# Kernel optimization log

Hardware: AMD Instinct MI355X
Metric: run time of the kernel (lower is better)

## Reference

```python
import jax, jax.numpy as jnp
import numpy as np

N = 50000   # nodes
E = 800000  # edges (avg degree 16)
F = 64      # num_features (channels per irrep)
R = 8       # radial basis size
H = 64      # radial MLP hidden
S = 10      # num_species
NPATH = 5   # tensor-product paths: s*Y0->0, s*Y1->1, v*Y0->1, v.Y1->0, v x Y1->1
AVG_NEIGH = 16.0


def setup_inputs() -> dict:
    key = jax.random.key(0)
    ks = jax.random.split(key, 20)
    def w(k, shape, fan_in):
        return jax.random.normal(k, shape, dtype=jnp.float32) / np.sqrt(fan_in)
    return dict(
        vectors=jax.random.normal(ks[0], (E, 3), dtype=jnp.float32),
        node_feats_s=jax.random.normal(ks[1], (N, F), dtype=jnp.float32),
        node_feats_v=jax.random.normal(ks[2], (N, F, 3), dtype=jnp.float32),
        radial_embedding=jax.random.normal(ks[3], (E, R), dtype=jnp.float32),
        Wu_s=w(ks[7], (F, F), F), Wu_v=w(ks[8], (F, F), F),
        W_r1=w(ks[9], (R, H), R), W_r2=w(ks[10], (H, NPATH * F), H),
        Wd_s=w(ks[11], (F, F), F), Wd_v=w(ks[12], (F, F), F),
        w_sym_s=jax.random.normal(ks[13], (S, 3, F), dtype=jnp.float32),
        w_sym_v=jax.random.normal(ks[14], (S, 2, F), dtype=jnp.float32),
        WL_s=w(ks[15], (F, F), F), WL_v=w(ks[16], (F, F), F),
        W_skip_s=w(ks[17], (S, F, F), F), W_skip_v=w(ks[18], (S, F, F), F),
        W_out=w(ks[19], (F, 1), F),
        node_specie=jax.random.randint(ks[4], (N,), 0, S),
        senders=jax.random.randint(ks[5], (E,), 0, N),
        receivers=jax.random.randint(ks[6], (E,), 0, N),
    )


def reference(vectors, node_feats_s, node_feats_v, radial_embedding,
              Wu_s, Wu_v, W_r1, W_r2, Wd_s, Wd_v,
              w_sym_s, w_sym_v, WL_s, WL_v, W_skip_s, W_skip_v, W_out,
              node_specie, senders, receivers):
    n = node_feats_s.shape[0]
    # ---- self-connection: species-indexed linear (skip_tp), per-irrep channel mix
    sc_s = jnp.einsum('nf,nfg->ng', node_feats_s, W_skip_s[node_specie])
    sc_v = jnp.einsum('nfc,nfg->ngc', node_feats_v, W_skip_v[node_specie])
    # ---- InteractionBlock: linear up
    s = node_feats_s @ Wu_s                                  # [N,F]
    v = jnp.einsum('nfc,fg->ngc', node_feats_v, Wu_v)        # [N,F,3]
    # radial MLP -> per-edge, per-path, per-channel tensor-product weights
    h = jax.nn.silu(radial_embedding @ W_r1)
    w = (h @ W_r2).reshape(-1, NPATH, s.shape[1])            # [E,5,F]
    # spherical harmonics (l=1): unit edge vectors
    Y1 = vectors / (jnp.linalg.norm(vectors, axis=-1, keepdims=True) + 1e-9)  # [E,3]
    xs = s[senders]                                          # [E,F]
    xv = v[senders]                                          # [E,F,3]
    # CG tensor product paths (0e+1o) x (Y0+Y1) -> 0e + 1o
    m_s = w[:, 0] * xs + w[:, 3] * jnp.einsum('efc,ec->ef', xv, Y1)
    m_v = (w[:, 1, :, None] * xs[:, :, None] * Y1[:, None, :]
           + w[:, 2, :, None] * xv
           + w[:, 4, :, None] * jnp.cross(xv, Y1[:, None, :]))
    # scatter-sum aggregation over receivers
    agg_s = jax.ops.segment_sum(m_s, receivers, num_segments=n)
    agg_v = jax.ops.segment_sum(m_v, receivers, num_segments=n)
    # linear down to num_features * interaction_irreps
    s = agg_s @ Wd_s
    v = jnp.einsum('nfc,fg->ngc', agg_v, Wd_v)
    # epsilon is None -> divide by sqrt(avg_num_neighbors)
    inv = 1.0 / np.sqrt(AVG_NEIGH).astype(np.float32)
    s = s * inv
    v = v * inv
    # ---- EquivariantProductBasisBlock: symmetric contraction (correlation=2),
    # species-indexed per-channel weights over the symmetric CG basis
    ws = w_sym_s[node_specie]                                # [N,3,F]
    wv = w_sym_v[node_specie]                                # [N,2,F]
    ps = ws[:, 0] * s + ws[:, 1] * s * s + ws[:, 2] * jnp.sum(v * v, axis=-1)
    pv = wv[:, 0, :, None] * v + wv[:, 1, :, None] * (s[:, :, None] * v)
    # linear to num_features * hidden_irreps
    fs = ps @ WL_s
    fv = jnp.einsum('nfc,fg->ngc', pv, WL_v)
    # residual skip connection
    fs = fs + sc_s
    fv = fv + sc_v
    # ---- LinearReadoutBlock to output_irreps = '0e'
    node_outputs = fs @ W_out                                # [N,1]
    return node_outputs, fs, fv
```

## Files before the change

kernel.cpp:

```cpp
#include <hip/hip_runtime.h>
#include <stdint.h>

#define F 64
#define RDIM 8
#define HDIM 64
#define NPATH 5
#define EB 64
#define PADH 72
#define PADN 324
#define NSP 16
#define PB 72
#define NT 4

typedef _Float16 half8 __attribute__((ext_vector_type(8)));
typedef _Float16 half4 __attribute__((ext_vector_type(4)));
typedef float floatx4 __attribute__((ext_vector_type(4)));

__device__ inline half8 h8_from_f32(const float* p) {
    float4 a = ((const float4*)p)[0];
    float4 b = ((const float4*)p)[1];
    half8 h;
    h[0] = (_Float16)a.x; h[1] = (_Float16)a.y; h[2] = (_Float16)a.z; h[3] = (_Float16)a.w;
    h[4] = (_Float16)b.x; h[5] = (_Float16)b.y; h[6] = (_Float16)b.z; h[7] = (_Float16)b.w;
    return h;
}

__device__ inline half8 h8_from_f32_stride3(const float* p) {
    half8 h;
#pragma unroll
    for (int j = 0; j < 8; ++j) h[j] = (_Float16)p[j * 3];
    return h;
}

__device__ inline half8 h8_zero() {
    half8 h;
#pragma unroll
    for (int j = 0; j < 8; ++j) h[j] = (_Float16)0.f;
    return h;
}

__global__ __launch_bounds__(256) void k_pre(
    const float* __restrict__ nfs, const float* __restrict__ nfv,
    const float* __restrict__ Wus, const float* __restrict__ Wuv,
    half4* __restrict__ comb, int N)
{
    __shared__ float4 stage[4][F];
    const int wave = threadIdx.x >> 6, lane = threadIdx.x & 63;
    const int n = blockIdx.x * 4 + wave;
    const bool act = n < N;
    if (act) {
        float xs = nfs[(size_t)n * F + lane];
        const float* pv = nfv + ((size_t)n * F + lane) * 3;
        stage[wave][lane] = make_float4(xs, pv[0], pv[1], pv[2]);
    }
    __syncthreads();
    if (!act) return;
    float as = 0.f, a0 = 0.f, a1 = 0.f, a2 = 0.f;
#pragma unroll 8
    for (int f = 0; f < F; ++f) {
        float4 x = stage[wave][f];
        float ws = Wus[f * F + lane];
        float wv = Wuv[f * F + lane];
        as += x.x * ws; a0 += x.y * wv; a1 += x.z * wv; a2 += x.w * wv;
    }
    half4 o;
    o[0] = (_Float16)as; o[1] = (_Float16)a0; o[2] = (_Float16)a1; o[3] = (_Float16)a2;
    comb[(size_t)n * F + lane] = o;
}

__global__ __launch_bounds__(256) void k_hist(
    const int* __restrict__ recv, int* __restrict__ cnt, int E)
{
    int i = blockIdx.x * 256 + threadIdx.x;
    const int stride = gridDim.x * 256;
    for (; i < E; i += stride) atomicAdd(&cnt[recv[i]], 1);
}

__global__ __launch_bounds__(1024) void k_scanA(
    const int* __restrict__ cnt, int* __restrict__ bsum, int N)
{
    __shared__ int lsum[1024];
    const int tid = threadIdx.x;
    const int i = blockIdx.x * 1024 + tid;
    int x = (i < N) ? cnt[i] : 0;
    lsum[tid] = x;
    __syncthreads();
    for (int off = 512; off > 0; off >>= 1) {
        if (tid < off) lsum[tid] += lsum[tid + off];
        __syncthreads();
    }
    if (tid == 0) bsum[blockIdx.x] = lsum[0];
}

__global__ __launch_bounds__(64) void k_scanB(int* __restrict__ bsum, int nb)
{
    const int lane = threadIdx.x;
    int carry = 0;
    for (int base = 0; base < nb; base += 64) {
        const int idx = base + lane;
        int v = (idx < nb) ? bsum[idx] : 0;
        int incl = v;
#pragma unroll
        for (int off = 1; off < 64; off <<= 1) {
            int u = __shfl_up(incl, off, 64);
            if (lane >= off) incl += u;
        }
        int tot = __shfl(incl, 63, 64);
        if (idx < nb) bsum[idx] = incl - v + carry;
        carry += tot;
    }
}

__global__ __launch_bounds__(1024) void k_scanC(
    const int* __restrict__ cnt, const int* __restrict__ bsum,
    int* __restrict__ cursor, int N)
{
    __shared__ int lsum[1024];
    const int tid = threadIdx.x;
    const int i = blockIdx.x * 1024 + tid;
    int x = (i < N) ? cnt[i] : 0;
    lsum[tid] = x;
    __syncthreads();
    int acc = x;
    for (int off = 1; off < 1024; off <<= 1) {
        int add = (tid >= off) ? lsum[tid - off] : 0;
        __syncthreads();
        acc += add;
        lsum[tid] = acc;
        __syncthreads();
    }
    if (i < N) cursor[i] = acc - x + bsum[blockIdx.x];
}

__global__ __launch_bounds__(256) void k_scatter(
    const int* __restrict__ recv, const int* __restrict__ send,
    int* __restrict__ cursor, int* __restrict__ perm,
    int2* __restrict__ srsort, int E)
{
    int i = blockIdx.x * 256 + threadIdx.x;
    const int stride = gridDim.x * 256;
    for (; i < E; i += stride) {
        int r = recv[i];
        int p = atomicAdd(&cursor[r], 1);
        perm[p] = i;
        srsort[p] = make_int2(send[i], r);
    }
}

__global__ __launch_bounds__(256) void k_nhist(
    const int* __restrict__ specie, int* __restrict__ nbin, int N)
{
    __shared__ int lbin[NSP];
    const int tid = threadIdx.x;
    if (tid < NSP) lbin[tid] = 0;
    __syncthreads();
    const int i = blockIdx.x * 256 + tid;
    if (i < N) atomicAdd(&lbin[specie[i]], 1);
    __syncthreads();
    if (tid < NSP && lbin[tid] > 0) atomicAdd(&nbin[tid], lbin[tid]);
}

__global__ __launch_bounds__(64) void k_nscan(
    const int* __restrict__ nbin, int* __restrict__ ncur)
{
    if (threadIdx.x == 0) {
        int run = 0;
        for (int s = 0; s < NSP; ++s) {
            ncur[s] = run;
            run += ((nbin[s] + 63) >> 6) << 6;
        }
    }
}

__global__ __launch_bounds__(256) void k_nscatter(
    const int* __restrict__ specie, int* __restrict__ ncur,
    int* __restrict__ nperm, int N)
{
    __shared__ int lbin[NSP], lbase[NSP], lcur[NSP];
    const int tid = threadIdx.x;
    if (tid < NSP) { lbin[tid] = 0; lcur[tid] = 0; }
    __syncthreads();
    const int i = blockIdx.x * 256 + tid;
    int sp = -1;
    if (i < N) { sp = specie[i]; atomicAdd(&lbin[sp], 1); }
    __syncthreads();
    if (tid < NSP && lbin[tid] > 0) lbase[tid] = atomicAdd(&ncur[tid], lbin[tid]);
    __syncthreads();
    if (i < N) {
        int off = atomicAdd(&lcur[sp], 1);
        nperm[lbase[sp] + off] = i;
    }
}

__global__ __launch_bounds__(256, 3) void k_edge(
    const float* __restrict__ vecs, const float* __restrict__ re,
    const float* __restrict__ Wr1, const float* __restrict__ Wr2,
    const int* __restrict__ perm, const int2* __restrict__ srsort,
    const half4* __restrict__ comb,
    float* __restrict__ agg_s, float* __restrict__ agg_v, int E)
{
    __shared__ _Float16 h_lds[EB * PADH];
    __shared__ _Float16 w_lds[EB * PADN];
    const int tid = threadIdx.x;
    const int wave = tid >> 6, lane = tid & 63;
    const int l15 = lane & 15, lq = lane >> 4;

    half8 bfrag[5][2];
#pragma unroll
    for (int nt = 0; nt < 5; ++nt)
#pragma unroll
        for (int ks = 0; ks < 2; ++ks)
#pragma unroll
            for (int j = 0; j < 8; ++j) {
                int k = ks * 32 + lq * 8 + j;
                int n = wave * 80 + nt * 16 + l15;
                bfrag[nt][ks][j] = (_Float16)Wr2[k * (NPATH * F) + n];
            }

    float w1r[RDIM];
#pragma unroll
    for (int r = 0; r < RDIM; ++r) w1r[r] = Wr1[r * HDIM + lane];

    const int niter = (E + EB - 1) / EB;
    for (int it = blockIdx.x; it < niter; it += gridDim.x) {
        const int base = it * EB;
        const bool full = (base + EB <= E);

        if (full) {
            const int ew = base + wave * 16;
            int pm[16];
#pragma unroll
            for (int j = 0; j < 4; ++j)
                ((int4*)pm)[j] = ((const int4*)(perm + ew))[j];
            float4 ra[4], rb[4];
#pragma unroll
            for (int j = 0; j < 4; ++j) {
                const float4* rp = (const float4*)(re + (size_t)pm[j] * RDIM);
                ra[j] = rp[0]; rb[j] = rp[1];
            }
#pragma unroll
            for (int t = 0; t < 16; ++t) {
                float4 A = ra[t & 3], B = rb[t & 3];
                if (t < 12) {
                    const float4* rp = (const float4*)(re + (size_t)pm[t + 4] * RDIM);
                    ra[t & 3] = rp[0]; rb[t & 3] = rp[1];
                }
                float h = A.x * w1r[0] + A.y * w1r[1] + A.z * w1r[2] + A.w * w1r[3]
                        + B.x * w1r[4] + B.y * w1r[5] + B.z * w1r[6] + B.w * w1r[7];
                h = h / (1.f + __expf(-h));
                h_lds[(wave * 16 + t) * PADH + lane] = (_Float16)h;
            }
        } else {
            for (int t = 0; t < 16; ++t) {
                const int eloc = wave * 16 + t;
                const int e = base + eloc;
                float h = 0.f;
                if (e < E) {
                    const int pe = perm[e];
                    const float4* rp = (const float4*)(re + (size_t)pe * RDIM);
                    float4 A = rp[0], B = rp[1];
                    h = A.x * w1r[0] + A.y * w1r[1] + A.z * w1r[2] + A.w * w1r[3]
                      + B.x * w1r[4] + B.y * w1r[5] + B.z * w1r[6] + B.w * w1r[7];
                    h = h / (1.f + __expf(-h));
                }
                h_lds[eloc * PADH + lane] = (_Float16)h;
            }
        }
        __syncthreads();

        floatx4 c[4][5];
#pragma unroll
        for (int mt = 0; mt < 4; ++mt)
#pragma unroll
            for (int nt = 0; nt < 5; ++nt)
                c[mt][nt] = (floatx4){0.f, 0.f, 0.f, 0.f};
#pragma unroll
        for (int ks = 0; ks < 2; ++ks) {
            half8 a[4];
#pragma unroll
            for (int mt = 0; mt < 4; ++mt)
                a[mt] = *(const half8*)&h_lds[(mt * 16 + l15) * PADH + ks * 32 + lq * 8];
#pragma unroll
            for (int mt = 0; mt < 4; ++mt)
#pragma unroll
                for (int nt = 0; nt < 5; ++nt)
                    c[mt][nt] = __builtin_amdgcn_mfma_f32_16x16x32_f16(
                        a[mt], bfrag[nt][ks], c[mt][nt], 0, 0, 0);
        }
#pragma unroll
        for (int mt = 0; mt < 4; ++mt)
#pragma unroll
            for (int nt = 0; nt < 5; ++nt)
#pragma unroll
                for (int r = 0; r < 4; ++r) {
                    int row = mt * 16 + lq * 4 + r;
                    int col = wave * 80 + nt * 16 + l15;
                    w_lds[row * PADN + col] = (_Float16)c[mt][nt][r];
                }
        __syncthreads();

        if (full) {
            const int ew = base + wave * 16;
            int pm[16];
            int2 sr[16];
#pragma unroll
            for (int j = 0; j < 4; ++j)
                ((int4*)pm)[j] = ((const int4*)(perm + ew))[j];
#pragma unroll
            for (int j = 0; j < 8; ++j)
                ((int4*)sr)[j] = ((const int4*)(srsort + ew))[j];
            half4 gb[4];
            float vxr[4], vyr[4], vzr[4];
#pragma unroll
            for (int j = 0; j < 4; ++j) {
                gb[j] = comb[(size_t)sr[j].x * F + lane];
                const float* vp = vecs + (size_t)pm[j] * 3;
                vxr[j] = vp[0]; vyr[j] = vp[1]; vzr[j] = vp[2];
            }
            float accs = 0.f, acc0 = 0.f, acc1 = 0.f, acc2 = 0.f;
            int cur = sr[0].y;
#pragma unroll
            for (int t = 0; t < 16; ++t) {
                half4 g = gb[t & 3];
                float vx = vxr[t & 3], vy = vyr[t & 3], vz = vzr[t & 3];
                if (t < 12) {
                    gb[t & 3] = comb[(size_t)sr[t + 4].x * F + lane];
                    const float* vp = vecs + (size_t)pm[t + 4] * 3;
                    vxr[t & 3] = vp[0]; vyr[t & 3] = vp[1]; vzr[t & 3] = vp[2];
                }
                const int eloc = wave * 16 + t;
                float nrm = sqrtf(vx * vx + vy * vy + vz * vz);
                float inv = 1.f / (nrm + 1e-9f);
                float Yx = vx * inv, Yy = vy * inv, Yz = vz * inv;
                float w0  = (float)w_lds[eloc * PADN + 0 * F + lane];
                float w1p = (float)w_lds[eloc * PADN + 1 * F + lane];
                float w2p = (float)w_lds[eloc * PADN + 2 * F + lane];
                float w3p = (float)w_lds[eloc * PADN + 3 * F + lane];
                float w4p = (float)w_lds[eloc * PADN + 4 * F + lane];
                float xs = (float)g[0], x0 = (float)g[1], x1 = (float)g[2], x2 = (float)g[3];
                float dvY = x0 * Yx + x1 * Yy + x2 * Yz;
                float ms = w0 * xs + w3p * dvY;
                float m0 = w1p * xs * Yx + w2p * x0 + w4p * (x1 * Yz - x2 * Yy);
                float m1 = w1p * xs * Yy + w2p * x1 + w4p * (x2 * Yx - x0 * Yz);
                float m2 = w1p * xs * Yz + w2p * x2 + w4p * (x0 * Yy - x1 * Yx);
                if (sr[t].y != cur) {
                    float* asb = agg_s + (size_t)cur * F;
                    float* avb = agg_v + (size_t)cur * 3 * F;
                    unsafeAtomicAdd(&asb[lane], accs);
                    unsafeAtomicAdd(&avb[lane], acc0);
                    unsafeAtomicAdd(&avb[F + lane], acc1);
                    unsafeAtomicAdd(&avb[2 * F + lane], acc2);
                    accs = acc0 = acc1 = acc2 = 0.f;
                    cur = sr[t].y;
                }
                accs += ms; acc0 += m0; acc1 += m1; acc2 += m2;
            }
            {
                float* asb = agg_s + (size_t)cur * F;
                float* avb = agg_v + (size_t)cur * 3 * F;
                unsafeAtomicAdd(&asb[lane], accs);
                unsafeAtomicAdd(&avb[lane], acc0);
                unsafeAtomicAdd(&avb[F + lane], acc1);
                unsafeAtomicAdd(&avb[2 * F + lane], acc2);
            }
        } else {
            for (int t = 0; t < 16; ++t) {
                const int eloc = wave * 16 + t;
                const int e = base + eloc;
                if (e >= E) break;
                const int pe = perm[e];
                const int2 sr = srsort[e];
                const int snd = sr.x, rcv = sr.y;
                const float* vp = vecs + (size_t)pe * 3;
                float vx = vp[0], vy = vp[1], vz = vp[2];
                float nrm = sqrtf(vx * vx + vy * vy + vz * vz);
                float inv = 1.f / (nrm + 1e-9f);
                float Yx = vx * inv, Yy = vy * inv, Yz = vz * inv;
                half4 g = comb[(size_t)snd * F + lane];
                float w0  = (float)w_lds[eloc * PADN + 0 * F + lane];
                float w1p = (float)w_lds[eloc * PADN + 1 * F + lane];
                float w2p = (float)w_lds[eloc * PADN + 2 * F + lane];
                float w3p = (float)w_lds[eloc * PADN + 3 * F + lane];
                float w4p = (float)w_lds[eloc * PADN + 4 * F + lane];
                float xs = (float)g[0], x0 = (float)g[1], x1 = (float)g[2], x2 = (float)g[3];
                float dvY = x0 * Yx + x1 * Yy + x2 * Yz;
                float ms = w0 * xs + w3p * dvY;
                float m0 = w1p * xs * Yx + w2p * x0 + w4p * (x1 * Yz - x2 * Yy);
                float m1 = w1p * xs * Yy + w2p * x1 + w4p * (x2 * Yx - x0 * Yz);
                float m2 = w1p * xs * Yz + w2p * x2 + w4p * (x0 * Yy - x1 * Yx);
                float* asb = agg_s + (size_t)rcv * F;
                float* avb = agg_v + (size_t)rcv * 3 * F;
                unsafeAtomicAdd(&asb[lane], ms);
                unsafeAtomicAdd(&avb[lane], m0);
                unsafeAtomicAdd(&avb[F + lane], m1);
                unsafeAtomicAdd(&avb[2 * F + lane], m2);
            }
        }
    }
}

__global__ __launch_bounds__(256) void k_post_mfma(
    const float* __restrict__ agg_s, const float* __restrict__ agg_v,
    const float* __restrict__ nfs, const float* __restrict__ nfv,
    const float* __restrict__ Wds, const float* __restrict__ Wdv,
    const float* __restrict__ wss, const float* __restrict__ wsv,
    const float* __restrict__ WLs, const float* __restrict__ WLv,
    const float* __restrict__ Wsks, const float* __restrict__ Wskv,
    const float* __restrict__ Wout, const int* __restrict__ specie,
    const int* __restrict__ nperm,
    float* __restrict__ out0, float* __restrict__ out_fs,
    float* __restrict__ out_fv, int N)
{
    __shared__ _Float16 BT[6][64 * PB];
    __shared__ _Float16 P_lds[4][16 * PB];
    const int tid = threadIdx.x;
    const int wave = tid >> 6, lane = tid & 63;
    const int l15 = lane & 15, lq = lane >> 4;
    const int tb0 = blockIdx.x * 64;

    const int nfirst = nperm[tb0];
    const int sp = (nfirst < 0) ? 0 : specie[nfirst];

    {
        const float* srcs[6] = { Wds, Wdv,
                                 Wsks + (size_t)sp * F * F, Wskv + (size_t)sp * F * F,
                                 WLs, WLv };
#pragma unroll
        for (int m = 0; m < 6; ++m) {
            const float* W = srcs[m];
#pragma unroll
            for (int rep = 0; rep < 16; ++rep) {
                int id = rep * 256 + tid;
                int k = id >> 6, n = id & 63;
                BT[m][n * PB + k] = (_Float16)W[k * F + n];
            }
        }
    }
    __syncthreads();

    const int tb = tb0 + wave * 16;
    const int ndA = nperm[tb + l15];
    int ndr[4];
#pragma unroll
    for (int r = 0; r < 4; ++r) ndr[r] = nperm[tb + lq * 4 + r];

#define BFRAG(m, nt, ks) (*(const half8*)&BT[m][((nt) * 16 + l15) * PB + (ks) * 32 + lq * 8])

    floatx4 csk[4][NT];
#pragma unroll
    for (int q = 0; q < 4; ++q)
#pragma unroll
        for (int nt = 0; nt < NT; ++nt) csk[q][nt] = (floatx4){0.f, 0.f, 0.f, 0.f};
#pragma unroll
    for (int ks = 0; ks < 2; ++ks) {
        half8 a_s, a_v0, a_v1, a_v2;
        if (ndA >= 0) {
            a_s  = h8_from_f32(nfs + (size_t)ndA * F + ks * 32 + lq * 8);
            const float* vb = nfv + ((size_t)ndA * F + ks * 32 + lq * 8) * 3;
            a_v0 = h8_from_f32_stride3(vb + 0);
            a_v1 = h8_from_f32_stride3(vb + 1);
            a_v2 = h8_from_f32_stride3(vb + 2);
        } else {
            a_s = a_v0 = a_v1 = a_v2 = h8_zero();
        }
#pragma unroll
        for (int nt = 0; nt < NT; ++nt) {
            half8 bs = BFRAG(2, nt, ks);
            half8 bv = BFRAG(3, nt, ks);
            csk[0][nt] = __builtin_amdgcn_mfma_f32_16x16x32_f16(a_s,  bs, csk[0][nt], 0, 0, 0);
            csk[1][nt] = __builtin_amdgcn_mfma_f32_16x16x32_f16(a_v0, bv, csk[1][nt], 0, 0, 0);
            csk[2][nt] = __builtin_amdgcn_mfma_f32_16x16x32_f16(a_v1, bv, csk[2][nt], 0, 0, 0);
            csk[3][nt] = __builtin_amdgcn_mfma_f32_16x16x32_f16(a_v2, bv, csk[3][nt], 0, 0, 0);
        }
    }

    floatx4 cdn[4][NT];
#pragma unroll
    for (int q = 0; q < 4; ++q)
#pragma unroll
        for (int nt = 0; nt < NT; ++nt) cdn[q][nt] = (floatx4){0.f, 0.f, 0.f, 0.f};
#pragma unroll
    for (int ks = 0; ks < 2; ++ks) {
        half8 a_s, a_v0, a_v1, a_v2;
        if (ndA >= 0) {
            a_s  = h8_from_f32(agg_s + (size_t)ndA * F + ks * 32 + lq * 8);
            const float* vb = agg_v + (size_t)ndA * 3 * F + ks * 32 + lq * 8;
            a_v0 = h8_from_f32(vb);
            a_v1 = h8_from_f32(vb + F);
            a_v2 = h8_from_f32(vb + 2 * F);
        } else {
            a_s = a_v0 = a_v1 = a_v2 = h8_zero();
        }
#pragma unroll
        for (int nt = 0; nt < NT; ++nt) {
            half8 bs = BFRAG(0, nt, ks);
            half8 bv = BFRAG(1, nt, ks);
            cdn[0][nt] = __builtin_amdgcn_mfma_f32_16x16x32_f16(a_s,  bs, cdn[0][nt], 0, 0, 0);
            cdn[1][nt] = __builtin_amdgcn_mfma_f32_16x16x32_f16(a_v0, bv, cdn[1][nt], 0, 0, 0);
            cdn[2][nt] = __builtin_amdgcn_mfma_f32_16x16x32_f16(a_v1, bv, cdn[2][nt], 0, 0, 0);
            cdn[3][nt] = __builtin_amdgcn_mfma_f32_16x16x32_f16(a_v2, bv, cdn[3][nt], 0, 0, 0);
        }
    }

#pragma unroll
    for (int nt = 0; nt < NT; ++nt) {
        const int g = nt * 16 + l15;
        float a0 = wss[(sp * 3 + 0) * F + g];
        float a1 = wss[(sp * 3 + 1) * F + g];
        float a2 = wss[(sp * 3 + 2) * F + g];
        float b0 = wsv[(sp * 2 + 0) * F + g];
        float b1 = wsv[(sp * 2 + 1) * F + g];
#pragma unroll
        for (int r = 0; r < 4; ++r) {
            const float inv = 0.25f;
            float s2  = cdn[0][nt][r] * inv;
            float v20 = cdn[1][nt][r] * inv;
            float v21 = cdn[2][nt][r] * inv;
            float v22 = cdn[3][nt][r] * inv;
            cdn[0][nt][r] = a0 * s2 + a1 * s2 * s2
                          + a2 * (v20 * v20 + v21 * v21 + v22 * v22);
            cdn[1][nt][r] = b0 * v20 + b1 * s2 * v20;
            cdn[2][nt][r] = b0 * v21 + b1 * s2 * v21;
            cdn[3][nt][r] = b0 * v22 + b1 * s2 * v22;
        }
    }

#pragma unroll
    for (int q = 0; q < 4; ++q) {
#pragma unroll
        for (int nt = 0; nt < NT; ++nt)
#pragma unroll
            for (int r = 0; r < 4; ++r)
                P_lds[wave][(lq * 4 + r) * PB + nt * 16 + l15] = (_Float16)cdn[q][nt][r];
        __syncthreads();
        half8 ap0 = *(const half8*)&P_lds[wave][l15 * PB + 0 * 32 + lq * 8];
        half8 ap1 = *(const half8*)&P_lds[wave][l15 * PB + 1 * 32 + lq * 8];
        const int bm = (q == 0) ? 4 : 5;
#pragma unroll
        for (int nt = 0; nt < NT; ++nt) {
            csk[q][nt] = __builtin_amdgcn_mfma_f32_16x16x32_f16(ap0, BFRAG(bm, nt, 0), csk[q][nt], 0, 0, 0);
            csk[q][nt] = __builtin_amdgcn_mfma_f32_16x16x32_f16(ap1, BFRAG(bm, nt, 1), csk[q][nt], 0, 0, 0);
        }
        __syncthreads();
    }
#undef BFRAG

    float wo[NT];
#pragma unroll
    for (int nt = 0; nt < NT; ++nt) wo[nt] = Wout[nt * 16 + l15];
#pragma unroll
    for (int r = 0; r < 4; ++r) {
        const int nd = ndr[r];
        float po = 0.f;
        if (nd >= 0) {
#pragma unroll
            for (int nt = 0; nt < NT; ++nt) {
                const int g = nt * 16 + l15;
                float fs = csk[0][nt][r];
                out_fs[(size_t)nd * F + g] = fs;
                po += fs * wo[nt];
                float* fvp = out_fv + ((size_t)nd * F + g) * 3;
                fvp[0] = csk[1][nt][r];
                fvp[1] = csk[2][nt][r];
                fvp[2] = csk[3][nt][r];
            }
            po += __shfl_xor(po, 1, 64);
            po += __shfl_xor(po, 2, 64);
            po += __shfl_xor(po, 4, 64);
            po += __shfl_xor(po, 8, 64);
            if (l15 == 0) out0[nd] = po;
        }
    }
}

extern "C" void kernel_launch(void* const* d_in, const int* in_sizes, int n_in,
                              void* d_out, int out_size, void* d_ws, size_t ws_size,
                              hipStream_t stream)
{
    const float* vectors = (const float*)d_in[0];
    const float* nfs  = (const float*)d_in[1];
    const float* nfv  = (const float*)d_in[2];
    const float* re   = (const float*)d_in[3];
    const float* Wus  = (const float*)d_in[4];
    const float* Wuv  = (const float*)d_in[5];
    const float* Wr1  = (const float*)d_in[6];
    const float* Wr2  = (const float*)d_in[7];
    const float* Wds  = (const float*)d_in[8];
    const float* Wdv  = (const float*)d_in[9];
    const float* wss  = (const float*)d_in[10];
    const float* wsv  = (const float*)d_in[11];
    const float* WLs  = (const float*)d_in[12];
    const float* WLv  = (const float*)d_in[13];
    const float* Wsks = (const float*)d_in[14];
    const float* Wskv = (const float*)d_in[15];
    const float* Wout = (const float*)d_in[16];
    const int* specie    = (const int*)d_in[17];
    const int* senders   = (const int*)d_in[18];
    const int* receivers = (const int*)d_in[19];

    const int N = in_sizes[1] / F;
    const int E = in_sizes[18];

    const size_t NF = (size_t)N * F;
    const int NPAD_MAX = N + NSP * 64 + 64;
    half4* comb  = (half4*)d_ws;
    float* agg_s = (float*)((char*)d_ws + NF * sizeof(half4));
    float* agg_v = agg_s + NF;
    int*   perm  = (int*)(agg_v + 3 * NF);
    int2*  srsort = (int2*)(perm + E);
    int*   cnt    = (int*)(srsort + E);
    int*   nbin   = cnt + N;
    int*   ncur   = nbin + NSP;
    int*   cursor = ncur + NSP;
    int*   bsum   = cursor + N;
    int*   nperm  = bsum + 64;

    hipMemsetAsync(agg_s, 0, (size_t)4 * NF * sizeof(float), stream);
    hipMemsetAsync(cnt, 0, (size_t)(N + NSP) * sizeof(int), stream);
    hipMemsetAsync(nperm, 0xFF, (size_t)NPAD_MAX * sizeof(int), stream);

    const int nb = (N + 3) / 4;
    const int nbs = (N + 1023) / 1024;
    const int nb256 = (N + 255) / 256;
    const int nbp = (N + NSP * 64 + 63) / 64;

    k_pre<<<nb, 256, 0, stream>>>(nfs, nfv, Wus, Wuv, comb, N);
    k_hist<<<1024, 256, 0, stream>>>(receivers, cnt, E);
    k_scanA<<<nbs, 1024, 0, stream>>>(cnt, bsum, N);
    k_scanB<<<1, 64, 0, stream>>>(bsum, nbs);
    k_scanC<<<nbs, 1024, 0, stream>>>(cnt, bsum, cursor, N);
    k_scatter<<<1024, 256, 0, stream>>>(receivers, senders, cursor,
                                        perm, srsort, E);
    k_nhist<<<nb256, 256, 0, stream>>>(specie, nbin, N);
    k_nscan<<<1, 64, 0, stream>>>(nbin, ncur);
    k_nscatter<<<nb256, 256, 0, stream>>>(specie, ncur, nperm, N);
    k_edge<<<2048, 256, 0, stream>>>(vectors, re, Wr1, Wr2, perm, srsort,
                                     comb, agg_s, agg_v, E);
    float* out0   = (float*)d_out;
    float* out_fs = out0 + N;
    float* out_fv = out_fs + (size_t)N * F;
    k_post_mfma<<<nbp, 256, 0, stream>>>(agg_s, agg_v, nfs, nfv, Wds, Wdv,
                                         wss, wsv, WLs, WLv, Wsks, Wskv,
                                         Wout, specie, nperm,
                                         out0, out_fs, out_fv, N);
}
```

Before: 600.6 us.

## Use MFMA for the up-projection and fold the species sort into existing kernels

The per-node up-projection, previously a scalar FMA loop with one wave per node, becomes an MFMA f16 kernel. Each wave handles 16 nodes against transposed weights staged in LDS. The species histogram, scan and scatter, previously three separate launches, are folded into the receiver histogram, scanB and edge scatter kernels. This removes launch and small-kernel overhead. The fused node scatter assumes the fixed 1024-block grid covers all N nodes with one thread each.

```diff
diff --git a/kernel.cpp b/kernel.cpp
--- a/kernel.cpp
+++ b/kernel.cpp
@@ -39,41 +39,98 @@
     return h;
 }
 
-__global__ __launch_bounds__(256) void k_pre(
+__global__ __launch_bounds__(256) void k_pre_mfma(
     const float* __restrict__ nfs, const float* __restrict__ nfv,
     const float* __restrict__ Wus, const float* __restrict__ Wuv,
     half4* __restrict__ comb, int N)
 {
-    __shared__ float4 stage[4][F];
-    const int wave = threadIdx.x >> 6, lane = threadIdx.x & 63;
-    const int n = blockIdx.x * 4 + wave;
-    const bool act = n < N;
-    if (act) {
-        float xs = nfs[(size_t)n * F + lane];
-        const float* pv = nfv + ((size_t)n * F + lane) * 3;
-        stage[wave][lane] = make_float4(xs, pv[0], pv[1], pv[2]);
-    }
-    __syncthreads();
-    if (!act) return;
-    float as = 0.f, a0 = 0.f, a1 = 0.f, a2 = 0.f;
-#pragma unroll 8
-    for (int f = 0; f < F; ++f) {
-        float4 x = stage[wave][f];
-        float ws = Wus[f * F + lane];
-        float wv = Wuv[f * F + lane];
-        as += x.x * ws; a0 += x.y * wv; a1 += x.z * wv; a2 += x.w * wv;
-    }
-    half4 o;
-    o[0] = (_Float16)as; o[1] = (_Float16)a0; o[2] = (_Float16)a1; o[3] = (_Float16)a2;
-    comb[(size_t)n * F + lane] = o;
+    __shared__ _Float16 BT[2][64 * PB];
+    const int tid = threadIdx.x;
+    const int wave = tid >> 6, lane = tid & 63;
+    const int l15 = lane & 15, lq = lane >> 4;
+    const int tb0 = blockIdx.x * 64;
+
+    {
+        const float* srcs[2] = { Wus, Wuv };
+#pragma unroll
+        for (int m = 0; m < 2; ++m) {
+            const float* W = srcs[m];
+#pragma unroll
+            for (int rep = 0; rep < 16; ++rep) {
+                int id = rep * 256 + tid;
+                int k = id >> 6, n = id & 63;
+                BT[m][n * PB + k] = (_Float16)W[k * F + n];
+            }
+        }
+    }
+    __syncthreads();
+
+    const int tb = tb0 + wave * 16;
+    const int ndA = tb + l15;
+
+#define BFRAG(m, nt, ks) (*(const half8*)&BT[m][((nt) * 16 + l15) * PB + (ks) * 32 + lq * 8])
+
+    floatx4 c[4][NT];
+#pragma unroll
+    for (int q = 0; q < 4; ++q)
+#pragma unroll
+        for (int nt = 0; nt < NT; ++nt) c[q][nt] = (floatx4){0.f, 0.f, 0.f, 0.f};
+
+#pragma unroll
+    for (int ks = 0; ks < 2; ++ks) {
+        half8 a_s, a_v0, a_v1, a_v2;
+        if (ndA < N) {
+            a_s  = h8_from_f32(nfs + (size_t)ndA * F + ks * 32 + lq * 8);
+            const float* vb = nfv + ((size_t)ndA * F + ks * 32 + lq * 8) * 3;
+            a_v0 = h8_from_f32_stride3(vb + 0);
+            a_v1 = h8_from_f32_stride3(vb + 1);
+            a_v2 = h8_from_f32_stride3(vb + 2);
+        } else {
+            a_s = a_v0 = a_v1 = a_v2 = h8_zero();
+        }
+#pragma unroll
+        for (int nt = 0; nt < NT; ++nt) {
+            half8 bs = BFRAG(0, nt, ks);
+            half8 bv = BFRAG(1, nt, ks);
+            c[0][nt] = __builtin_amdgcn_mfma_f32_16x16x32_f16(a_s,  bs, c[0][nt], 0, 0, 0);
+            c[1][nt] = __builtin_amdgcn_mfma_f32_16x16x32_f16(a_v0, bv, c[1][nt], 0, 0, 0);
+            c[2][nt] = __builtin_amdgcn_mfma_f32_16x16x32_f16(a_v1, bv, c[2][nt], 0, 0, 0);
+            c[3][nt] = __builtin_amdgcn_mfma_f32_16x16x32_f16(a_v2, bv, c[3][nt], 0, 0, 0);
+        }
+    }
+#undef BFRAG
+
+#pragma unroll
+    for (int r = 0; r < 4; ++r) {
+        const int nd = tb + lq * 4 + r;
+        if (nd < N) {
+#pragma unroll
+            for (int nt = 0; nt < NT; ++nt) {
+                half4 o;
+                o[0] = (_Float16)c[0][nt][r];
+                o[1] = (_Float16)c[1][nt][r];
+                o[2] = (_Float16)c[2][nt][r];
+                o[3] = (_Float16)c[3][nt][r];
+                comb[(size_t)nd * F + nt * 16 + l15] = o;
+            }
+        }
+    }
 }
 
 __global__ __launch_bounds__(256) void k_hist(
-    const int* __restrict__ recv, int* __restrict__ cnt, int E)
-{
-    int i = blockIdx.x * 256 + threadIdx.x;
+    const int* __restrict__ recv, int* __restrict__ cnt, int E,
+    const int* __restrict__ specie, int* __restrict__ nbin, int N)
+{
+    __shared__ int lbin[NSP];
+    const int tid = threadIdx.x;
+    if (tid < NSP) lbin[tid] = 0;
+    __syncthreads();
+    const int i0 = blockIdx.x * 256 + tid;
     const int stride = gridDim.x * 256;
-    for (; i < E; i += stride) atomicAdd(&cnt[recv[i]], 1);
+    for (int e = i0; e < E; e += stride) atomicAdd(&cnt[recv[e]], 1);
+    for (int n = i0; n < N; n += stride) atomicAdd(&lbin[specie[n]], 1);
+    __syncthreads();
+    if (tid < NSP && lbin[tid] > 0) atomicAdd(&nbin[tid], lbin[tid]);
 }
 
 __global__ __launch_bounds__(1024) void k_scanA(
@@ -92,7 +149,9 @@
     if (tid == 0) bsum[blockIdx.x] = lsum[0];
 }
 
-__global__ __launch_bounds__(64) void k_scanB(int* __restrict__ bsum, int nb)
+__global__ __launch_bounds__(64) void k_scanB(
+    int* __restrict__ bsum, int nb,
+    const int* __restrict__ nbin, int* __restrict__ ncur)
 {
     const int lane = threadIdx.x;
     int carry = 0;
@@ -108,6 +167,13 @@
         int tot = __shfl(incl, 63, 64);
         if (idx < nb) bsum[idx] = incl - v + carry;
         carry += tot;
+    }
+    if (lane == 0) {
+        int run = 0;
+        for (int s = 0; s < NSP; ++s) {
+            ncur[s] = run;
+            run += ((nbin[s] + 63) >> 6) << 6;
+        }
     }
 }
 
@@ -135,60 +201,30 @@
 __global__ __launch_bounds__(256) void k_scatter(
     const int* __restrict__ recv, const int* __restrict__ send,
     int* __restrict__ cursor, int* __restrict__ perm,
-    int2* __restrict__ srsort, int E)
-{
-    int i = blockIdx.x * 256 + threadIdx.x;
-    const int stride = gridDim.x * 256;
-    for (; i < E; i += stride) {
-        int r = recv[i];
-        int p = atomicAdd(&cursor[r], 1);
-        perm[p] = i;
-        srsort[p] = make_int2(send[i], r);
-    }
-}
-
-__global__ __launch_bounds__(256) void k_nhist(
-    const int* __restrict__ specie, int* __restrict__ nbin, int N)
-{
-    __shared__ int lbin[NSP];
-    const int tid = threadIdx.x;
-    if (tid < NSP) lbin[tid] = 0;
-    __syncthreads();
-    const int i = blockIdx.x * 256 + tid;
-    if (i < N) atomicAdd(&lbin[specie[i]], 1);
-    __syncthreads();
-    if (tid < NSP && lbin[tid] > 0) atomicAdd(&nbin[tid], lbin[tid]);
-}
-
-__global__ __launch_bounds__(64) void k_nscan(
-    const int* __restrict__ nbin, int* __restrict__ ncur)
-{
-    if (threadIdx.x == 0) {
-        int run = 0;
-        for (int s = 0; s < NSP; ++s) {
-            ncur[s] = run;
-            run += ((nbin[s] + 63) >> 6) << 6;
-        }
-    }
-}
-
-__global__ __launch_bounds__(256) void k_nscatter(
+    int2* __restrict__ srsort, int E,
     const int* __restrict__ specie, int* __restrict__ ncur,
     int* __restrict__ nperm, int N)
 {
     __shared__ int lbin[NSP], lbase[NSP], lcur[NSP];
     const int tid = threadIdx.x;
+    const int i0 = blockIdx.x * 256 + tid;
+    const int stride = gridDim.x * 256;
+    for (int e = i0; e < E; e += stride) {
+        int r = recv[e];
+        int p = atomicAdd(&cursor[r], 1);
+        perm[p] = e;
+        srsort[p] = make_int2(send[e], r);
+    }
     if (tid < NSP) { lbin[tid] = 0; lcur[tid] = 0; }
     __syncthreads();
-    const int i = blockIdx.x * 256 + tid;
     int sp = -1;
-    if (i < N) { sp = specie[i]; atomicAdd(&lbin[sp], 1); }
+    if (i0 < N) { sp = specie[i0]; atomicAdd(&lbin[sp], 1); }
     __syncthreads();
     if (tid < NSP && lbin[tid] > 0) lbase[tid] = atomicAdd(&ncur[tid], lbin[tid]);
     __syncthreads();
-    if (i < N) {
+    if (i0 < N) {
         int off = atomicAdd(&lcur[sp], 1);
-        nperm[lbase[sp] + off] = i;
+        nperm[lbase[sp] + off] = i0;
     }
 }
 
@@ -619,21 +655,17 @@
     hipMemsetAsync(cnt, 0, (size_t)(N + NSP) * sizeof(int), stream);
     hipMemsetAsync(nperm, 0xFF, (size_t)NPAD_MAX * sizeof(int), stream);
 
-    const int nb = (N + 3) / 4;
+    const int nb64 = (N + 63) / 64;
     const int nbs = (N + 1023) / 1024;
-    const int nb256 = (N + 255) / 256;
     const int nbp = (N + NSP * 64 + 63) / 64;
 
-    k_pre<<<nb, 256, 0, stream>>>(nfs, nfv, Wus, Wuv, comb, N);
-    k_hist<<<1024, 256, 0, stream>>>(receivers, cnt, E);
+    k_pre_mfma<<<nb64, 256, 0, stream>>>(nfs, nfv, Wus, Wuv, comb, N);
+    k_hist<<<1024, 256, 0, stream>>>(receivers, cnt, E, specie, nbin, N);
     k_scanA<<<nbs, 1024, 0, stream>>>(cnt, bsum, N);
-    k_scanB<<<1, 64, 0, stream>>>(bsum, nbs);
+    k_scanB<<<1, 64, 0, stream>>>(bsum, nbs, nbin, ncur);
     k_scanC<<<nbs, 1024, 0, stream>>>(cnt, bsum, cursor, N);
     k_scatter<<<1024, 256, 0, stream>>>(receivers, senders, cursor,
-                                        perm, srsort, E);
-    k_nhist<<<nb256, 256, 0, stream>>>(specie, nbin, N);
-    k_nscan<<<1, 64, 0, stream>>>(nbin, ncur);
-    k_nscatter<<<nb256, 256, 0, stream>>>(specie, ncur, nperm, N);
+                                        perm, srsort, E, specie, ncur, nperm, N);
     k_edge<<<2048, 256, 0, stream>>>(vectors, re, Wr1, Wr2, perm, srsort,
                                      comb, agg_s, agg_v, E);
     float* out0   = (float*)d_out;
```

New measurement: 551.9 us. 8.1% less time.
